# Kernel tuning notes

Measured on AMD Instinct MI355X. Metric: run time of the kernel, lower is better.

## Reference

```python
import jax, jax.numpy as jnp
import numpy as np

MIN_CONF = 0.05          # min_confidence
NMS_IOU = 0.4            # per-class nms iou threshold
POST_IOU = 0.65          # post (cross-class, per-image) nms iou threshold
MAX_OUT = 1000           # nms_max_output_size (also the 'top 1000 boxes' cap)


def _corners(boxes):
    # boxes: [..., 4] (cx, cy, w, h) -> (y1, x1, y2, x2); image w=h=1 since
    # NormalizeBoxes is called without a shape kwarg in the original layer.
    cx, cy, w, h = jnp.moveaxis(boxes, -1, 0)
    return jnp.stack([cy - h / 2, cx - w / 2, cy + h / 2, cx + w / 2], axis=-1)


def _iou_matrix(b):
    # b: [K, 4] (y1, x1, y2, x2) -> [K, K] pairwise IoU
    y1, x1, y2, x2 = b[:, 0], b[:, 1], b[:, 2], b[:, 3]
    area = (y2 - y1) * (x2 - x1)
    ih = jnp.clip(jnp.minimum(y2[:, None], y2[None, :]) - jnp.maximum(y1[:, None], y1[None, :]), 0.0)
    iw = jnp.clip(jnp.minimum(x2[:, None], x2[None, :]) - jnp.maximum(x1[:, None], x1[None, :]), 0.0)
    inter = ih * iw
    union = area[:, None] + area[None, :] - inter
    return inter / jnp.maximum(union, 1e-8)


def _greedy_nms(b, valid, thresh):
    # b: [K,4] corner boxes sorted by descending score; valid: [K] bool.
    # Greedy NMS identical to tf.image.non_max_suppression (suppress IoU > thresh).
    iou = _iou_matrix(b)
    K = b.shape[0]
    idx = jnp.arange(K)
    def body(i, supp):
        active = valid[i] & jnp.logical_not(supp[i])
        return supp | (active & (iou[i] > thresh) & (idx > i))
    supp = jax.lax.fori_loop(0, K, body, jnp.zeros(K, dtype=bool))
    return valid & jnp.logical_not(supp)


def _forward(cls_pred, boxes):
    B, N, C = cls_pred.shape
    K1 = MAX_OUT
    corners = _corners(boxes)                                 # [B, N, 4]

    # --- stage 1: confidence filter + per-(image,class) NMS -----------------
    scores = jnp.transpose(cls_pred, (0, 2, 1))               # [B, C, N]
    masked = jnp.where(scores >= MIN_CONF, scores, -1.0)
    s1, i1 = jax.lax.top_k(masked, K1)                        # [B, C, K1], top-1000 cap
    v1 = s1 >= MIN_CONF
    b1 = jnp.take_along_axis(corners[:, None], i1[..., None], axis=2)  # [B, C, K1, 4]
    keep1 = jax.vmap(lambda bb, vv: _greedy_nms(bb, vv, NMS_IOU))(
        b1.reshape(B * C, K1, 4), v1.reshape(B * C, K1)).reshape(B, C, K1)

    # --- stage 2: per-image cross-class post-NMS ----------------------------
    s2 = jnp.where(keep1, s1, -1.0).reshape(B, C * K1)
    cls_ids = jnp.broadcast_to(jnp.arange(C)[None, :, None], (B, C, K1)).reshape(B, C * K1)
    b2 = b1.reshape(B, C * K1, 4)
    i2 = i1.reshape(B, C * K1)

    K2 = MAX_OUT
    s2t, sel = jax.lax.top_k(s2, K2)                          # [B, K2]
    v2 = s2t >= MIN_CONF
    b2t = jnp.take_along_axis(b2, sel[..., None], axis=1)     # [B, K2, 4]
    cls_t = jnp.take_along_axis(cls_ids, sel, axis=1)         # [B, K2]
    orig_t = jnp.take_along_axis(i2, sel, axis=1)             # [B, K2] anchor index
    keep2 = jax.vmap(lambda bb, vv: _greedy_nms(bb, vv, POST_IOU))(b2t, v2)

    # --- compact kept detections to the front, pad with zeros ---------------
    order = jnp.argsort(jnp.logical_not(keep2).astype(jnp.int32), axis=1)  # stable
    keep_s = jnp.take_along_axis(keep2, order, axis=1)
    conf = jnp.where(keep_s, jnp.take_along_axis(s2t, order, axis=1), 0.0)
    cls_f = jnp.where(keep_s, jnp.take_along_axis(cls_t, order, axis=1), 0).astype(jnp.float32)
    oidx = jnp.take_along_axis(orig_t, order, axis=1)
    raw = jnp.take_along_axis(boxes, oidx[..., None], axis=1)  # original (cx,cy,w,h)
    raw = jnp.where(keep_s[..., None], raw, 0.0)
    out = jnp.concatenate([raw, cls_f[..., None], conf[..., None]], axis=-1)  # [B, K2, 6]
    return jax.lax.stop_gradient(out)


def setup_inputs() -> dict:
    key = jax.random.key(0)
    k1, k2 = jax.random.split(key)
    B, N, C = 8, 100000, 10
    cls_pred = jax.random.uniform(k1, (B, N, C), dtype=jnp.float32)
    boxes = jax.random.uniform(k2, (B, N, 4), dtype=jnp.float32)  # (cx, cy, w, h)
    return {"cls_pred": cls_pred, "boxes": boxes}


def reference(cls_pred, boxes):
    return _forward(cls_pred, boxes)
```

## Files before the change

kernel.cpp:

```cpp
#include <hip/hip_runtime.h>
#include <stdint.h>

typedef unsigned int u32;
typedef unsigned long long u64;

#define B_ 8
#define N_ 100000
#define C_ 10
#define K1_ 1000
#define N2_ (C_ * K1_)
#define NBIN 4096
#define CAP 4096
#define CAP_C 2048
#define SEGROWS 256
#define MIN_CONF_F 0.05f
#define NMS_IOU_F 0.4f
#define POST_IOU_F 0.65f
#define T0_F 0.985f

#define TOTAL_F4 (B_ * N_ * C_ / 4)
#define CBLK 512
#define LCAP 1024

#define NTILE 136
#define NB_ 34
#define TPB_ 4

static __device__ __forceinline__ u32 next_pow2_ge(u32 x, u32 lo, u32 hi) {
  u32 n = lo;
  while (n < x && n < hi) n <<= 1;
  return n;
}

#define TILE_ID(rt, w) ((rt) * 16 - (((rt) * ((rt) - 1)) >> 1) + ((w) - (rt)))

__global__ void k_init(u32* __restrict__ cnt, u32* __restrict__ flag) {
  int t = threadIdx.x;
  if (t < B_ * C_) { cnt[t] = 0; flag[t] = 0; }
}

__global__ __launch_bounds__(256) void k_compact(const float* __restrict__ cls,
                                                 u64* __restrict__ cand,
                                                 u32* __restrict__ cnt,
                                                 u32* __restrict__ flag) {
  __shared__ u32 lcnt[B_ * C_];
  __shared__ u32 sbase[B_ * C_];
  __shared__ u32 ltot;
  __shared__ u32 lovf;
  __shared__ u64 ekey[LCAP];
  __shared__ u32 emeta[LCAP];

  const int tid = threadIdx.x;
  if (tid < B_ * C_) lcnt[tid] = 0;
  if (tid == 0) { ltot = 0; lovf = 0; }
  __syncthreads();

  const u32 lo = (u32)blockIdx.x * ((TOTAL_F4 + CBLK - 1) / CBLK);
  u32 hi = lo + ((TOTAL_F4 + CBLK - 1) / CBLK);
  if (hi > TOTAL_F4) hi = TOTAL_F4;

  const float4* p4 = (const float4*)cls;
  for (u32 f = lo + tid; f < hi; f += 256) {
    float4 v = p4[f];
    u32 e = f * 4u;
    float vs[4] = {v.x, v.y, v.z, v.w};
#pragma unroll
    for (int j = 0; j < 4; ++j) {
      float s = vs[j];
      if (s >= T0_F) {
        u32 g = e + (u32)j;
        u32 gi = g / (u32)C_;
        u32 c = g - gi * (u32)C_;
        u32 bi = gi / (u32)N_;
        u32 i = gi - bi * (u32)N_;
        u32 slice = bi * (u32)C_ + c;
        u32 rank = atomicAdd(&lcnt[slice], 1u);
        u32 pos = atomicAdd(&ltot, 1u);
        if (pos < LCAP) {
          ekey[pos] = ((u64)__float_as_uint(s) << 32) | (u32)(~i);
          emeta[pos] = (slice << 16) | rank;
        } else {
          lovf = 1;
        }
      }
    }
  }
  __syncthreads();

  if (lovf) {
    if (tid < B_ * C_) flag[tid] = 1;
  }
  if (tid < B_ * C_) {
    u32 n = lcnt[tid];
    sbase[tid] = n ? atomicAdd(&cnt[tid], n) : 0u;
  }
  __syncthreads();

  u32 tot = ltot;
  if (tot > LCAP) tot = LCAP;
  for (u32 p = tid; p < tot; p += 256) {
    u32 mta = emeta[p];
    u32 slice = mta >> 16;
    u32 rank = mta & 0xFFFFu;
    u32 dst = sbase[slice] + rank;
    if (dst < CAP_C) cand[(size_t)slice * CAP_C + dst] = ekey[p];
  }
}

__device__ __forceinline__ void bitonic_sort_desc(u64* buf, u32 n, int tid,
                                                  int bd) {
  for (u32 kk = 2; kk <= n; kk <<= 1) {
    for (u32 j = kk >> 1; j > 0; j >>= 1) {
      for (u32 t = tid; t < (n >> 1); t += bd) {
        u32 i = ((t & ~(j - 1)) << 1) | (t & (j - 1));
        u32 l = i | j;
        u64 a = buf[i], bb = buf[l];
        bool desc = ((i & kk) == 0);
        if (desc ? (a < bb) : (a > bb)) { buf[i] = bb; buf[l] = a; }
      }
      __syncthreads();
    }
  }
}

__global__ __launch_bounds__(1024) void k_sel(const u64* __restrict__ cand,
                                              const u32* __restrict__ cnt,
                                              u32* __restrict__ flag,
                                              float* __restrict__ score1,
                                              int* __restrict__ idx1) {
  const int slice = blockIdx.x;
  const int tid = threadIdx.x;
  __shared__ u64 buf[CAP_C];

  u32 m = cnt[slice];
  if (flag[slice] || m < (u32)K1_ || m > (u32)CAP_C) {
    if (tid == 0) flag[slice] = 1;
    return;
  }
  const u32 n = next_pow2_ge(m, 1024u, (u32)CAP_C);

  for (u32 i = tid; i < n; i += 1024)
    buf[i] = (i < m) ? cand[(size_t)slice * CAP_C + i] : 0ull;
  __syncthreads();

  bitonic_sort_desc(buf, n, tid, 1024);

  if (tid < K1_) {
    u64 e = buf[tid];
    u32 k = (u32)(e >> 32);
    score1[slice * K1_ + tid] = __uint_as_float(k);
    idx1[slice * K1_ + tid] = (int)(~(u32)e);
  }
}

__global__ __launch_bounds__(256) void k_topk1_fb(const float* __restrict__ cls,
                                                  const u32* __restrict__ flag,
                                                  float* __restrict__ score1,
                                                  int* __restrict__ idx1) {
  const int slice = blockIdx.x;
  if (!flag[slice]) return;
  const int b = slice / C_, c = slice % C_;
  const int tid = threadIdx.x, bd = blockDim.x;

  __shared__ u32 hist[NBIN];
  __shared__ u64 buf[CAP];
  __shared__ int sh_b1;
  __shared__ u32 sh_base, sh_T, sh_cnt;

  for (int i = tid; i < NBIN; i += bd) hist[i] = 0;
  __syncthreads();
  for (int i = tid; i < N_; i += bd) {
    float s = cls[((size_t)b * N_ + i) * C_ + c];
    if (s >= MIN_CONF_F) atomicAdd(&hist[__float_as_uint(s) >> 19], 1u);
  }
  __syncthreads();
  if (tid == 0) {
    u32 cum = 0; int b1 = -1; u32 base = 0;
    for (int bin = NBIN - 1; bin >= 0; --bin) {
      cum += hist[bin];
      if (cum >= (u32)K1_) { b1 = bin; base = cum - hist[bin]; break; }
    }
    sh_b1 = b1; sh_base = base;
    if (b1 < 0) sh_T = 0;
  }
  __syncthreads();
  const int b1 = sh_b1;

  if (b1 >= 0) {
    const u32 base = sh_base;
    for (int i = tid; i < NBIN; i += bd) hist[i] = 0;
    __syncthreads();
    for (int i = tid; i < N_; i += bd) {
      float s = cls[((size_t)b * N_ + i) * C_ + c];
      if (s >= MIN_CONF_F) {
        u32 k = __float_as_uint(s);
        if ((int)(k >> 19) == b1) atomicAdd(&hist[(k >> 7) & 0xFFFu], 1u);
      }
    }
    __syncthreads();
    if (tid == 0) {
      u32 cum = base;
      u32 T = ((u32)b1) << 19;
      for (int bin = NBIN - 1; bin >= 0; --bin) {
        cum += hist[bin];
        if (cum >= (u32)K1_) { T = (((u32)b1) << 19) | (((u32)bin) << 7); break; }
      }
      sh_T = T;
    }
    __syncthreads();
  }

  if (tid == 0) sh_cnt = 0;
  __syncthreads();
  const u32 T = sh_T;
  for (int i = tid; i < N_; i += bd) {
    float s = cls[((size_t)b * N_ + i) * C_ + c];
    if (s >= MIN_CONF_F) {
      u32 k = __float_as_uint(s);
      if (k >= T) {
        u32 pos = atomicAdd(&sh_cnt, 1u);
        if (pos < CAP) buf[pos] = ((u64)k << 32) | (u32)(~(u32)i);
      }
    }
  }
  __syncthreads();
  u32 m = sh_cnt; if (m > CAP) m = CAP;
  for (int i = tid; i < CAP; i += bd)
    if ((u32)i >= m) buf[i] = 0ull;
  __syncthreads();

  for (u32 kk = 2; kk <= CAP; kk <<= 1) {
    for (u32 j = kk >> 1; j > 0; j >>= 1) {
      for (u32 i = tid; i < CAP; i += bd) {
        u32 l = i ^ j;
        if (l > i) {
          u64 a = buf[i], bb = buf[l];
          bool desc = ((i & kk) == 0);
          if (desc ? (a < bb) : (a > bb)) { buf[i] = bb; buf[l] = a; }
        }
      }
      __syncthreads();
    }
  }

  for (int p = tid; p < K1_; p += bd) {
    u64 e = buf[p];
    u32 k = (u32)(e >> 32);
    float s; int oi;
    if (k == 0) { s = -1.0f; oi = 0; }
    else { s = __uint_as_float(k); oi = (int)(~(u32)e); }
    score1[slice * K1_ + p] = s;
    idx1[slice * K1_ + p] = oi;
  }
}


__global__ __launch_bounds__(256) void k_nms_prep(const float* __restrict__ scores_all,
                                                  const int* __restrict__ origs_all,
                                                  const float* __restrict__ boxes,
                                                  int bdiv,
                                                  float4* __restrict__ cor,
                                                  float* __restrict__ areag) {
  const int slice = blockIdx.x;
  const int b = slice / bdiv;
  const float* scores = scores_all + slice * K1_;
  const int* origs = origs_all + slice * K1_;
  const float* bb = boxes + (size_t)b * N_ * 4;
  for (int p = threadIdx.x; p < 1024; p += 256) {
    float s = (p < K1_) ? scores[p] : -1.0f;
    bool v = (s >= MIN_CONF_F);
    float cx = 0.f, cy = 0.f, w = 0.f, h = 0.f;
    if (v) {
      const float4 bp = *(const float4*)(bb + (size_t)origs[p] * 4);
      cx = bp.x; cy = bp.y; w = bp.z; h = bp.w;
    }
    float y1 = cy - h * 0.5f, x1 = cx - w * 0.5f;
    float y2 = cy + h * 0.5f, x2 = cx + w * 0.5f;
    cor[(slice << 10) + p] = make_float4(y1, x1, y2, x2);
    areag[(slice << 10) + p] = (y2 - y1) * (x2 - x1);
  }
}

__global__ __launch_bounds__(256) void k_nms_build(const float4* __restrict__ cor,
                                                   const float* __restrict__ areag,
                                                   float thr,
                                                   u64* __restrict__ maskg) {
  __shared__ float4 box4[1024];
  __shared__ float area[1024];
  const int blk = blockIdx.x;
  const int slice = blk / NB_;
  const int sub = blk - slice * NB_;
  const int tid = threadIdx.x, wave = tid >> 6, lane = tid & 63;

  for (int p = tid; p < 1024; p += 256) {
    box4[p] = cor[(slice << 10) + p];
    area[p] = areag[(slice << 10) + p];
  }
  __syncthreads();

  const float cf = thr;
  const float cnext = __uint_as_float(__float_as_uint(cf) + 1u);
  const double M = ((double)cf + (double)cnext) * 0.5;
  const bool strict = ((__float_as_uint(cf) & 1u) == 0u);

  u64* mg = maskg + (size_t)slice * (NTILE * 64);

  for (int k = wave; k < TPB_; k += 4) {
    const int tt = sub * TPB_ + k;
    if (tt >= NTILE) break;
    int rt = 0, bse = 0;
    while (tt >= bse + (16 - rt)) { bse += 16 - rt; ++rt; }
    const int w = rt + (tt - bse);
    const int row = (rt << 6) | lane;

    const float4 ib = box4[row];
    const float ia = area[row];
    const float4* jcol = &box4[w << 6];
    u32 mhi = 0, mlo = 0;
#pragma unroll 8
    for (int j = 63; j >= 32; --j) {
      const float4 jb = jcol[j];
      const float ja = (jb.z - jb.x) * (jb.w - jb.y);
      float ih = fminf(ib.z, jb.z) - fmaxf(ib.x, jb.x); ih = fmaxf(ih, 0.0f);
      float iw_ = fminf(ib.w, jb.w) - fmaxf(ib.y, jb.y); iw_ = fmaxf(iw_, 0.0f);
      float inter = ih * iw_;
      float den = fmaxf((ia + ja) - inter, 1e-8f);
      bool p_ = strict ? ((double)inter > M * (double)den)
                       : ((double)inter >= M * (double)den);
      mhi = (mhi << 1) | (p_ ? 1u : 0u);
    }
#pragma unroll 8
    for (int j = 31; j >= 0; --j) {
      const float4 jb = jcol[j];
      const float ja = (jb.z - jb.x) * (jb.w - jb.y);
      float ih = fminf(ib.z, jb.z) - fmaxf(ib.x, jb.x); ih = fmaxf(ih, 0.0f);
      float iw_ = fminf(ib.w, jb.w) - fmaxf(ib.y, jb.y); iw_ = fmaxf(iw_, 0.0f);
      float inter = ih * iw_;
      float den = fmaxf((ia + ja) - inter, 1e-8f);
      bool p_ = strict ? ((double)inter > M * (double)den)
                       : ((double)inter >= M * (double)den);
      mlo = (mlo << 1) | (p_ ? 1u : 0u);
    }
    u64 m = ((u64)mhi << 32) | (u64)mlo;
    if (w == rt) m &= (lane == 63) ? 0ull : (~0ull << (lane + 1));
    mg[(tt << 6) + lane] = m;
  }
}

__device__ void scan_core(const u64* __restrict__ mg,
                          const float* __restrict__ scores,
                          u64* __restrict__ keepb) {
  const int tid = threadIdx.x, wv = tid >> 6, lane = tid & 63;

  float s = (tid < K1_) ? scores[tid] : -1.0f;
  const u64 myvalid = __ballot(s >= MIN_CONF_F);

  u64 ext_partial = 0;

#pragma unroll 1
  for (int g = 0; g < 16; ++g) {
    u64 Tg = 0ull;
    if (g <= wv) Tg = mg[(TILE_ID(g, wv) << 6) + lane];
    const u64 nz = __ballot(Tg != 0ull);
    if (wv == g) {
      u64 ext = ext_partial;
      for (int off = 1; off < 64; off <<= 1) {
        u32 lo = (u32)__shfl_xor((int)(u32)ext, off, 64);
        u32 hi = (u32)__shfl_xor((int)(u32)(ext >> 32), off, 64);
        ext |= ((u64)hi << 32) | lo;
      }
      const u32 tlo = (u32)Tg, thi = (u32)(Tg >> 32);
      u64 rem = myvalid & ~ext;
      u64 cand = rem & nz;
      while (cand) {
        int i = __ffsll((long long)cand) - 1;
        cand &= cand - 1;
        if ((rem >> i) & 1ull) {
          u32 rlo = __builtin_amdgcn_readlane(tlo, i);
          u32 rhi = __builtin_amdgcn_readlane(thi, i);
          u64 row = ((u64)rhi << 32) | rlo;
          rem &= ~row;
          cand &= ~row;
        }
      }
      if (lane == 0) keepb[g] = rem;
    }
    __syncthreads();
    if (wv > g) {
      u64 kg = keepb[g];
      if ((kg >> lane) & 1ull) ext_partial |= Tg;
    }
  }
}

__global__ __launch_bounds__(1024) void k_nms_scan1(const u64* __restrict__ maskg,
                                                    const float* __restrict__ score1,
                                                    int* __restrict__ keep1) {
  __shared__ u64 keepb[16];
  const int slice = blockIdx.x;
  scan_core(maskg + (size_t)slice * (NTILE * 64), score1 + slice * K1_, keepb);
  __syncthreads();
  const int p = threadIdx.x;
  if (p < K1_)
    keep1[slice * K1_ + p] = (int)((keepb[p >> 6] >> (p & 63)) & 1ull);
}

__global__ __launch_bounds__(1024) void k_nms_scan2(const u64* __restrict__ maskg,
                                                    const float* __restrict__ sel_score,
                                                    const int* __restrict__ sel_cls,
                                                    const int* __restrict__ sel_orig,
                                                    const float* __restrict__ boxes,
                                                    float* __restrict__ out) {
  __shared__ u64 keepb[16];
  __shared__ short ord[K1_];
  __shared__ int lbase[17];
  __shared__ int ordc;
  const int b = blockIdx.x;
  const int tid = threadIdx.x;
  scan_core(maskg + (size_t)b * (NTILE * 64), sel_score + b * K1_, keepb);
  __syncthreads();

  if (tid == 0) {
    int acc = 0;
    for (int wdx = 0; wdx < 16; ++wdx) {
      lbase[wdx] = acc;
      acc += __popcll(keepb[wdx]);
    }
    lbase[16] = acc;
    ordc = acc;
  }
  __syncthreads();
  if (tid < 16) {
    u64 m = keepb[tid];
    int base = lbase[tid];
    while (m) {
      int bit = __ffsll((long long)m) - 1;
      ord[base++] = (short)((tid << 6) | bit);
      m &= m - 1;
    }
  }
  __syncthreads();

  for (int t = tid; t < K1_ * 6; t += 1024) out[(size_t)b * K1_ * 6 + t] = 0.0f;
  __syncthreads();

  const int cnt = ordc;
  for (int q = tid; q < cnt; q += 1024) {
    int p = ord[q];
    int oi = sel_orig[b * K1_ + p];
    const float4 bp = *(const float4*)(boxes + ((size_t)b * N_ + oi) * 4);
    float* o = out + ((size_t)b * K1_ + q) * 6;
    o[0] = bp.x; o[1] = bp.y; o[2] = bp.z; o[3] = bp.w;
    o[4] = (float)sel_cls[b * K1_ + p];
    o[5] = sel_score[b * K1_ + p];
  }
}

__device__ __forceinline__ void nms_run(const float* __restrict__ scores,
                                        const int* __restrict__ origs,
                                        const float* __restrict__ boxesB,
                                        float thr,
                                        float4* box4, float* area,
                                        u64* mask, u64* validw, u64* keepw) {
  const int tid = threadIdx.x;
  const int wave = tid >> 6, lane = tid & 63;

  {
    const int p = tid;
    float s = (p < K1_) ? scores[p] : -1.0f;
    bool v = (s >= MIN_CONF_F);
    float cx = 0.f, cy = 0.f, w = 0.f, h = 0.f;
    if (v) {
      const float4 bp = *(const float4*)(boxesB + (size_t)origs[p] * 4);
      cx = bp.x; cy = bp.y; w = bp.z; h = bp.w;
    }
    float y1 = cy - h * 0.5f, x1 = cx - w * 0.5f;
    float y2 = cy + h * 0.5f, x2 = cx + w * 0.5f;
    box4[p] = make_float4(y1, x1, y2, x2);
    area[p] = (y2 - y1) * (x2 - x1);
    u64 mb = __ballot(v);
    if (lane == 0) validw[wave] = mb;
  }
  __syncthreads();

  const float cf = thr;
  const float cnext = __uint_as_float(__float_as_uint(cf) + 1u);
  const double M = ((double)cf + (double)cnext) * 0.5;
  const bool strict = ((__float_as_uint(cf) & 1u) == 0u);

  const int ss = wave & 3, qq = wave >> 2;
  int col;
  if (qq == 0) col = ss;
  else if (qq == 1) col = 7 - ss;
  else if (qq == 2) col = 8 + ss;
  else col = 15 - ss;

  u64 vw = validw[tid & 15];
  u64 supp = 0;

  for (int seg = 0; seg < 4; ++seg) {
    const int ibase = seg * SEGROWS;
    const int lim = (K1_ - ibase < SEGROWS) ? (K1_ - ibase) : SEGROWS;
    const int rtg0 = ibase >> 6;
    int ntile = col - rtg0 + 1;
    if (ntile < 0) ntile = 0;
    if (ntile > 4) ntile = 4;

    if (ntile > 0) {
      float4 ib[4];
      float ia[4];
#pragma unroll
      for (int r = 0; r < 4; ++r) {
        if (r < ntile) {
          const int i = ibase + (r << 6) + lane;
          ib[r] = box4[i];
          ia[r] = area[i];
        }
      }
      u32 mhi[4] = {0, 0, 0, 0}, mlo[4] = {0, 0, 0, 0};
      const float4* jcol = &box4[col << 6];

      for (int j = 63; j >= 32; --j) {
        const float4 jb = jcol[j];
        const float ja = (jb.z - jb.x) * (jb.w - jb.y);
#pragma unroll
        for (int r = 0; r < 4; ++r) {
          if (r < ntile) {
            float ih = fminf(ib[r].z, jb.z) - fmaxf(ib[r].x, jb.x);
            ih = fmaxf(ih, 0.0f);
            float iw_ = fminf(ib[r].w, jb.w) - fmaxf(ib[r].y, jb.y);
            iw_ = fmaxf(iw_, 0.0f);
            float inter = ih * iw_;
            float den = fmaxf((ia[r] + ja) - inter, 1e-8f);
            bool p_ = strict ? ((double)inter > M * (double)den)
                             : ((double)inter >= M * (double)den);
            mhi[r] = (mhi[r] << 1) | (p_ ? 1u : 0u);
          }
        }
      }
      for (int j = 31; j >= 0; --j) {
        const float4 jb = jcol[j];
        const float ja = (jb.z - jb.x) * (jb.w - jb.y);
#pragma unroll
        for (int r = 0; r < 4; ++r) {
          if (r < ntile) {
            float ih = fminf(ib[r].z, jb.z) - fmaxf(ib[r].x, jb.x);
            ih = fmaxf(ih, 0.0f);
            float iw_ = fminf(ib[r].w, jb.w) - fmaxf(ib[r].y, jb.y);
            iw_ = fmaxf(iw_, 0.0f);
            float inter = ih * iw_;
            float den = fmaxf((ia[r] + ja) - inter, 1e-8f);
            bool p_ = strict ? ((double)inter > M * (double)den)
                             : ((double)inter >= M * (double)den);
            mlo[r] = (mlo[r] << 1) | (p_ ? 1u : 0u);
          }
        }
      }
#pragma unroll
      for (int r = 0; r < 4; ++r) {
        if (r < ntile) {
          u64 m = ((u64)mhi[r] << 32) | (u64)mlo[r];
          if (rtg0 + r == col)
            m &= (lane == 63) ? 0ull : (~0ull << (lane + 1));
          const int il = (r << 6) | lane;
          mask[il * 16 + (col ^ (il & 15))] = m;
        }
      }
    }
    __syncthreads();

    if (tid < 64) {
      const int l = tid & 15;
      u64 r0 = 0, r1 = 0, r2 = 0, r3 = 0;
      if (l >= ((ibase + 0) >> 6)) r0 = mask[0 * 16 + (l ^ 0)];
      if (l >= ((ibase + 1) >> 6)) r1 = mask[1 * 16 + (l ^ 1)];
      if (l >= ((ibase + 2) >> 6)) r2 = mask[2 * 16 + (l ^ 2)];
      if (l >= ((ibase + 3) >> 6)) r3 = mask[3 * 16 + (l ^ 3)];
      for (int il = 0; il < lim; il += 4) {
        const int i0 = ibase + il;
        const int n0 = (il + 4 < lim) ? il + 4 : il;
        const int n1 = (il + 5 < lim) ? il + 5 : il;
        const int n2 = (il + 6 < lim) ? il + 6 : il;
        const int n3 = (il + 7 < lim) ? il + 7 : il;
        u64 m0 = r0, m1 = r1, m2 = r2, m3 = r3;
        r0 = (l >= ((ibase + n0) >> 6)) ? mask[n0 * 16 + (l ^ (n0 & 15))] : 0ull;
        r1 = (l >= ((ibase + n1) >> 6)) ? mask[n1 * 16 + (l ^ (n1 & 15))] : 0ull;
        r2 = (l >= ((ibase + n2) >> 6)) ? mask[n2 * 16 + (l ^ (n2 & 15))] : 0ull;
        r3 = (l >= ((ibase + n3) >> 6)) ? mask[n3 * 16 + (l ^ (n3 & 15))] : 0ull;
        bool a;
        a = (tid == (i0 >> 6)) && (((vw & ~supp) >> (i0 & 63)) & 1ull);
        if (__any(a)) supp |= m0;
        a = (tid == ((i0 + 1) >> 6)) && (((vw & ~supp) >> ((i0 + 1) & 63)) & 1ull);
        if (__any(a)) supp |= m1;
        a = (tid == ((i0 + 2) >> 6)) && (((vw & ~supp) >> ((i0 + 2) & 63)) & 1ull);
        if (__any(a)) supp |= m2;
        a = (tid == ((i0 + 3) >> 6)) && (((vw & ~supp) >> ((i0 + 3) & 63)) & 1ull);
        if (__any(a)) supp |= m3;
      }
    }
    __syncthreads();
  }

  if (tid < 16) keepw[tid] = vw & ~supp;
}

__global__ __launch_bounds__(1024) void k_nms1(const float* __restrict__ boxes,
                                               const float* __restrict__ score1,
                                               const int* __restrict__ idx1,
                                               int* __restrict__ keep1) {
  __shared__ float4 box4[1024];
  __shared__ float area[1024];
  __shared__ u64 mask[SEGROWS * 16];
  __shared__ u64 validw[16], keepw[16];

  const int slice = blockIdx.x;
  const int b = slice / C_;
  nms_run(score1 + slice * K1_, idx1 + slice * K1_,
          boxes + (size_t)b * N_ * 4, NMS_IOU_F,
          box4, area, mask, validw, keepw);
  __syncthreads();

  const int p = threadIdx.x;
  if (p < K1_)
    keep1[slice * K1_ + p] = (int)((keepw[p >> 6] >> (p & 63)) & 1ull);
}

__global__ __launch_bounds__(1024) void k_nms2_out(const float* __restrict__ boxes,
                                                   const float* __restrict__ sel_score,
                                                   const int* __restrict__ sel_cls,
                                                   const int* __restrict__ sel_orig,
                                                   float* __restrict__ out) {
  __shared__ float4 box4[1024];
  __shared__ float area[1024];
  __shared__ u64 mask[SEGROWS * 16];
  __shared__ u64 validw[16], keepw[16];
  __shared__ short ord[K1_];
  __shared__ int lbase[17];
  __shared__ int ordc;

  const int b = blockIdx.x;
  const int tid = threadIdx.x;
  nms_run(sel_score + b * K1_, sel_orig + b * K1_,
          boxes + (size_t)b * N_ * 4, POST_IOU_F,
          box4, area, mask, validw, keepw);
  __syncthreads();

  if (tid == 0) {
    int acc = 0;
    for (int wdx = 0; wdx < 16; ++wdx) {
      lbase[wdx] = acc;
      acc += __popcll(keepw[wdx]);
    }
    lbase[16] = acc;
    ordc = acc;
  }
  __syncthreads();
  if (tid < 16) {
    u64 m = keepw[tid];
    int base = lbase[tid];
    while (m) {
      int bit = __ffsll((long long)m) - 1;
      ord[base++] = (short)((tid << 6) | bit);
      m &= m - 1;
    }
  }
  __syncthreads();

  for (int t = tid; t < K1_ * 6; t += 1024) out[(size_t)b * K1_ * 6 + t] = 0.0f;
  __syncthreads();

  const int cnt = ordc;
  for (int q = tid; q < cnt; q += 1024) {
    int p = ord[q];
    int oi = sel_orig[b * K1_ + p];
    const float4 bp = *(const float4*)(boxes + ((size_t)b * N_ + oi) * 4);
    float* o = out + ((size_t)b * K1_ + q) * 6;
    o[0] = bp.x; o[1] = bp.y; o[2] = bp.z; o[3] = bp.w;
    o[4] = (float)sel_cls[b * K1_ + p];
    o[5] = sel_score[b * K1_ + p];
  }
}

__device__ __forceinline__ void suffix_select(const u32* __restrict__ hist,
                                              u32* __restrict__ aux,
                                              u32 base, u32 K,
                                              int* out_bin, u32* out_next) {
  const int t = threadIdx.x;
  u32 h0 = hist[4 * t], h1 = hist[4 * t + 1];
  u32 h2 = hist[4 * t + 2], h3 = hist[4 * t + 3];
  aux[t] = h0 + h1 + h2 + h3;
  __syncthreads();
  for (int off = 1; off < 1024; off <<= 1) {
    u32 v = aux[t] + ((t + off < 1024) ? aux[t + off] : 0u);
    __syncthreads();
    aux[t] = v;
    __syncthreads();
  }
  if (t == 0 && base + aux[0] < K) { *out_bin = -1; *out_next = base; }
  u32 up = (t < 1023) ? aux[t + 1] : 0u;
  u32 s3 = h3 + up;
  u32 s2 = h2 + s3;
  u32 s1 = h1 + s2;
  u32 s0 = h0 + s1;
  u32 c0 = base + s0, c1 = base + s1, c2 = base + s2, c3 = base + s3;
  u32 c4 = base + up;
  if (c0 >= K && c1 < K) { *out_bin = 4 * t;     *out_next = c1; }
  if (c1 >= K && c2 < K) { *out_bin = 4 * t + 1; *out_next = c2; }
  if (c2 >= K && c3 < K) { *out_bin = 4 * t + 2; *out_next = c3; }
  if (c3 >= K && c4 < K) { *out_bin = 4 * t + 3; *out_next = c4; }
  __syncthreads();
}

__global__ __launch_bounds__(1024) void k_topk2(const float* __restrict__ score1,
                                                const int* __restrict__ idx1,
                                                const int* __restrict__ keep1,
                                                float* __restrict__ sel_score,
                                                int* __restrict__ sel_cls,
                                                int* __restrict__ sel_orig) {
  const int b = blockIdx.x;
  const int tid = threadIdx.x;

  __shared__ u32 hist[NBIN];
  __shared__ u32 aux[1024];
  __shared__ u64 buf[CAP];
  __shared__ int sh_bin;
  __shared__ u32 sh_next;
  __shared__ u32 sh_T, sh_cnt;

  for (int i = tid; i < NBIN; i += 1024) hist[i] = 0;
  __syncthreads();
  for (int f = tid; f < N2_; f += 1024) {
    if (keep1[b * N2_ + f])
      atomicAdd(&hist[__float_as_uint(score1[b * N2_ + f]) >> 19], 1u);
  }
  __syncthreads();
  suffix_select(hist, aux, 0u, (u32)K1_, &sh_bin, &sh_next);
  const int b1 = sh_bin;
  const u32 base = sh_next;

  if (b1 >= 0) {
    for (int i = tid; i < NBIN; i += 1024) hist[i] = 0;
    if (tid == 0) sh_bin = -2;
    __syncthreads();
    for (int f = tid; f < N2_; f += 1024) {
      if (keep1[b * N2_ + f]) {
        u32 k = __float_as_uint(score1[b * N2_ + f]);
        if ((int)(k >> 19) == b1) atomicAdd(&hist[(k >> 7) & 0xFFFu], 1u);
      }
    }
    __syncthreads();
    suffix_select(hist, aux, base, (u32)K1_, &sh_bin, &sh_next);
    if (tid == 0) {
      int b2 = sh_bin;
      sh_T = (b2 >= 0) ? ((((u32)b1) << 19) | (((u32)b2) << 7))
                       : (((u32)b1) << 19);
    }
  } else {
    if (tid == 0) sh_T = 0;
  }
  if (tid == 0) sh_cnt = 0;
  __syncthreads();

  const u32 T = sh_T;
  for (int f = tid; f < N2_; f += 1024) {
    if (keep1[b * N2_ + f]) {
      u32 k = __float_as_uint(score1[b * N2_ + f]);
      if (k >= T) {
        u32 pos = atomicAdd(&sh_cnt, 1u);
        if (pos < CAP) buf[pos] = ((u64)k << 32) | (u32)(~(u32)f);
      }
    }
  }
  __syncthreads();
  u32 m = sh_cnt; if (m > CAP) m = CAP;
  const u32 n = next_pow2_ge(m, 1024u, (u32)CAP);
  for (u32 i = tid; i < n; i += 1024)
    if (i >= m) buf[i] = 0ull;
  __syncthreads();

  bitonic_sort_desc(buf, n, tid, 1024);

  if (tid < K1_) {
    u64 e = buf[tid];
    u32 k = (u32)(e >> 32);
    float s; int cls, orig;
    if (k == 0) { s = -1.0f; cls = 0; orig = 0; }
    else {
      s = __uint_as_float(k);
      u32 f = ~(u32)e;
      cls = (int)(f / K1_);
      int slot = (int)(f - (u32)cls * K1_);
      orig = idx1[(b * C_ + cls) * K1_ + slot];
    }
    sel_score[b * K1_ + tid] = s;
    sel_cls[b * K1_ + tid] = cls;
    sel_orig[b * K1_ + tid] = orig;
  }
}

extern "C" void kernel_launch(void* const* d_in, const int* in_sizes, int n_in,
                              void* d_out, int out_size, void* d_ws, size_t ws_size,
                              hipStream_t stream) {
  const float* cls = (const float*)d_in[0];
  const float* boxes = (const float*)d_in[1];
  float* out = (float*)d_out;

  char* ws = (char*)d_ws;
  float* score1    = (float*)(ws);
  int*   idx1      = (int*)(ws + 320000);
  int*   keep1     = (int*)(ws + 640000);
  float* sel_score = (float*)(ws + 960000);
  int*   sel_cls   = (int*)(ws + 992000);
  int*   sel_orig  = (int*)(ws + 1024000);
  u32*   cnt       = (u32*)(ws + 1056000);
  u32*   flag      = (u32*)(ws + 1056320);
  u64*   cand      = (u64*)(ws + 1056640);
  u64*    mask1 = (u64*)(ws + 2367488);
  u64*    mask2 = (u64*)(ws + 7938048);
  float4* cor1  = (float4*)(ws + 8495104);
  float*  area1 = (float*)(ws + 9805824);
  float4* cor2  = (float4*)(ws + 10133504);
  float*  area2 = (float*)(ws + 10264576);
  const size_t WS_NEED = 10297344;

  hipLaunchKernelGGL(k_init, dim3(1), dim3(256), 0, stream, cnt, flag);
  hipLaunchKernelGGL(k_compact, dim3(CBLK), dim3(256), 0, stream,
                     cls, cand, cnt, flag);
  hipLaunchKernelGGL(k_sel, dim3(B_ * C_), dim3(1024), 0, stream,
                     cand, cnt, flag, score1, idx1);
  hipLaunchKernelGGL(k_topk1_fb, dim3(B_ * C_), dim3(256), 0, stream,
                     cls, flag, score1, idx1);

  if (ws_size >= WS_NEED) {
    hipLaunchKernelGGL(k_nms_prep, dim3(B_ * C_), dim3(256), 0, stream,
                       score1, idx1, boxes, C_, cor1, area1);
    hipLaunchKernelGGL(k_nms_build, dim3(B_ * C_ * NB_), dim3(256), 0, stream,
                       cor1, area1, NMS_IOU_F, mask1);
    hipLaunchKernelGGL(k_nms_scan1, dim3(B_ * C_), dim3(1024), 0, stream,
                       mask1, score1, keep1);
    hipLaunchKernelGGL(k_topk2, dim3(B_), dim3(1024), 0, stream,
                       score1, idx1, keep1, sel_score, sel_cls, sel_orig);
    hipLaunchKernelGGL(k_nms_prep, dim3(B_), dim3(256), 0, stream,
                       sel_score, sel_orig, boxes, 1, cor2, area2);
    hipLaunchKernelGGL(k_nms_build, dim3(B_ * NB_), dim3(256), 0, stream,
                       cor2, area2, POST_IOU_F, mask2);
    hipLaunchKernelGGL(k_nms_scan2, dim3(B_), dim3(1024), 0, stream,
                       mask2, sel_score, sel_cls, sel_orig, boxes, out);
  } else {
    hipLaunchKernelGGL(k_nms1, dim3(B_ * C_), dim3(1024), 0, stream,
                       boxes, score1, idx1, keep1);
    hipLaunchKernelGGL(k_topk2, dim3(B_), dim3(1024), 0, stream,
                       score1, idx1, keep1, sel_score, sel_cls, sel_orig);
    hipLaunchKernelGGL(k_nms2_out, dim3(B_), dim3(1024), 0, stream,
                       boxes, sel_score, sel_cls, sel_orig, out);
  }
}
```

Measured before the change: 233.1 us.

## Drop init and prep kernels via per-block segments and fused box prep

Compaction now writes each block's candidates to a private segment with a per-block prefix header instead of using global atomics, so the separate init kernel goes away. The selection kernel gathers those segments with a prefix scan and falls back to the histogram top-k path inside the same kernel, so the fallback launch is removed. Box corner and area computation is fused into the mask-build kernel, which removes the prep launches and their intermediate buffers. The cost is that the gather in k_sel is serial per thread, and every build block recomputes the corners.

```diff
diff --git a/kernel.cpp b/kernel.cpp
--- a/kernel.cpp
+++ b/kernel.cpp
@@ -21,6 +21,7 @@
 #define TOTAL_F4 (B_ * N_ * C_ / 4)
 #define CBLK 512
 #define LCAP 1024
+#define HDRW 84
 
 #define NTILE 136
 #define NB_ 34
@@ -34,28 +35,23 @@
 
 #define TILE_ID(rt, w) ((rt) * 16 - (((rt) * ((rt) - 1)) >> 1) + ((w) - (rt)))
 
-__global__ void k_init(u32* __restrict__ cnt, u32* __restrict__ flag) {
-  int t = threadIdx.x;
-  if (t < B_ * C_) { cnt[t] = 0; flag[t] = 0; }
-}
-
 __global__ __launch_bounds__(256) void k_compact(const float* __restrict__ cls,
                                                  u64* __restrict__ cand,
-                                                 u32* __restrict__ cnt,
-                                                 u32* __restrict__ flag) {
+                                                 u32* __restrict__ hdr) {
   __shared__ u32 lcnt[B_ * C_];
-  __shared__ u32 sbase[B_ * C_];
+  __shared__ u32 lpre[B_ * C_ + 1];
   __shared__ u32 ltot;
   __shared__ u32 lovf;
   __shared__ u64 ekey[LCAP];
   __shared__ u32 emeta[LCAP];
 
   const int tid = threadIdx.x;
+  const u32 bk = blockIdx.x;
   if (tid < B_ * C_) lcnt[tid] = 0;
   if (tid == 0) { ltot = 0; lovf = 0; }
   __syncthreads();
 
-  const u32 lo = (u32)blockIdx.x * ((TOTAL_F4 + CBLK - 1) / CBLK);
+  const u32 lo = bk * ((TOTAL_F4 + CBLK - 1) / CBLK);
   u32 hi = lo + ((TOTAL_F4 + CBLK - 1) / CBLK);
   if (hi > TOTAL_F4) hi = TOTAL_F4;
 
@@ -87,24 +83,30 @@
   }
   __syncthreads();
 
-  if (lovf) {
-    if (tid < B_ * C_) flag[tid] = 1;
-  }
-  if (tid < B_ * C_) {
-    u32 n = lcnt[tid];
-    sbase[tid] = n ? atomicAdd(&cnt[tid], n) : 0u;
-  }
-  __syncthreads();
+  if (tid < B_ * C_) lpre[tid + 1] = lcnt[tid];
+  if (tid == 0) lpre[0] = 0;
+  __syncthreads();
+  for (int off = 1; off < B_ * C_; off <<= 1) {
+    u32 v = 0;
+    const bool act = (tid >= off && tid <= B_ * C_);
+    if (act) v = lpre[tid - off];
+    __syncthreads();
+    if (act) lpre[tid] += v;
+    __syncthreads();
+  }
 
   u32 tot = ltot;
   if (tot > LCAP) tot = LCAP;
+  u64* seg = cand + (size_t)bk * LCAP;
   for (u32 p = tid; p < tot; p += 256) {
     u32 mta = emeta[p];
     u32 slice = mta >> 16;
     u32 rank = mta & 0xFFFFu;
-    u32 dst = sbase[slice] + rank;
-    if (dst < CAP_C) cand[(size_t)slice * CAP_C + dst] = ekey[p];
-  }
+    u32 dst = lpre[slice] + rank;
+    if (dst < LCAP) seg[dst] = ekey[p];
+  }
+  if (tid <= B_ * C_) hdr[bk * HDRW + tid] = lpre[tid];
+  if (tid == 0) hdr[bk * HDRW + 81] = lovf;
 }
 
 __device__ __forceinline__ void bitonic_sort_desc(u64* buf, u32 n, int tid,
@@ -123,49 +125,72 @@
   }
 }
 
-__global__ __launch_bounds__(1024) void k_sel(const u64* __restrict__ cand,
-                                              const u32* __restrict__ cnt,
-                                              u32* __restrict__ flag,
+__global__ __launch_bounds__(1024) void k_sel(const float* __restrict__ cls,
+                                              const u64* __restrict__ cand,
+                                              const u32* __restrict__ hdr,
                                               float* __restrict__ score1,
                                               int* __restrict__ idx1) {
   const int slice = blockIdx.x;
   const int tid = threadIdx.x;
-  __shared__ u64 buf[CAP_C];
-
-  u32 m = cnt[slice];
-  if (flag[slice] || m < (u32)K1_ || m > (u32)CAP_C) {
-    if (tid == 0) flag[slice] = 1;
-    return;
-  }
-  const u32 n = next_pow2_ge(m, 1024u, (u32)CAP_C);
-
-  for (u32 i = tid; i < n; i += 1024)
-    buf[i] = (i < m) ? cand[(size_t)slice * CAP_C + i] : 0ull;
-  __syncthreads();
-
-  bitonic_sort_desc(buf, n, tid, 1024);
-
-  if (tid < K1_) {
-    u64 e = buf[tid];
-    u32 k = (u32)(e >> 32);
-    score1[slice * K1_ + tid] = __uint_as_float(k);
-    idx1[slice * K1_ + tid] = (int)(~(u32)e);
-  }
-}
-
-__global__ __launch_bounds__(256) void k_topk1_fb(const float* __restrict__ cls,
-                                                  const u32* __restrict__ flag,
-                                                  float* __restrict__ score1,
-                                                  int* __restrict__ idx1) {
-  const int slice = blockIdx.x;
-  if (!flag[slice]) return;
-  const int b = slice / C_, c = slice % C_;
-  const int tid = threadIdx.x, bd = blockDim.x;
+  const int bd = 1024;
 
   __shared__ u32 hist[NBIN];
   __shared__ u64 buf[CAP];
   __shared__ int sh_b1;
-  __shared__ u32 sh_base, sh_T, sh_cnt;
+  __shared__ u32 sh_base, sh_T, sh_cnt, sh_ovf;
+
+  u32* cnts = hist;
+  u32* starts = hist + 512;
+  u32* pre = hist + 1024;
+
+  if (tid == 0) sh_ovf = 0;
+  __syncthreads();
+  if (tid < CBLK) {
+    const u32* h = hdr + (size_t)tid * HDRW;
+    u32 a = h[slice], b2 = h[slice + 1];
+    starts[tid] = a;
+    cnts[tid] = b2 - a;
+    pre[tid + 1] = b2 - a;
+    if (h[81]) sh_ovf = 1;
+  }
+  if (tid == 0) pre[0] = 0;
+  __syncthreads();
+  for (int off = 1; off < CBLK; off <<= 1) {
+    u32 v = 0;
+    const bool act = (tid >= off && tid <= CBLK);
+    if (act) v = pre[tid - off];
+    __syncthreads();
+    if (act) pre[tid] += v;
+    __syncthreads();
+  }
+  const u32 m = pre[CBLK];
+  const bool fast = (sh_ovf == 0) && m >= (u32)K1_ && m <= (u32)CAP_C;
+
+  if (fast) {
+    if (tid < CBLK) {
+      u32 n = cnts[tid];
+      u32 base = pre[tid];
+      const u64* src = cand + (size_t)tid * LCAP + starts[tid];
+      for (u32 r = 0; r < n; ++r) buf[base + r] = src[r];
+    }
+    __syncthreads();
+    const u32 nn = next_pow2_ge(m, 1024u, (u32)CAP_C);
+    for (u32 i2 = tid; i2 < nn; i2 += bd)
+      if (i2 >= m) buf[i2] = 0ull;
+    __syncthreads();
+
+    bitonic_sort_desc(buf, nn, tid, bd);
+
+    if (tid < K1_) {
+      u64 e = buf[tid];
+      u32 k = (u32)(e >> 32);
+      score1[slice * K1_ + tid] = __uint_as_float(k);
+      idx1[slice * K1_ + tid] = (int)(~(u32)e);
+    }
+    return;
+  }
+
+  const int b = slice / C_, c = slice % C_;
 
   for (int i = tid; i < NBIN; i += bd) hist[i] = 0;
   __syncthreads();
@@ -224,9 +249,9 @@
     }
   }
   __syncthreads();
-  u32 m = sh_cnt; if (m > CAP) m = CAP;
+  u32 mm = sh_cnt; if (mm > CAP) mm = CAP;
   for (int i = tid; i < CAP; i += bd)
-    if ((u32)i >= m) buf[i] = 0ull;
+    if ((u32)i >= mm) buf[i] = 0ull;
   __syncthreads();
 
   for (u32 kk = 2; kk <= CAP; kk <<= 1) {
@@ -234,9 +259,9 @@
       for (u32 i = tid; i < CAP; i += bd) {
         u32 l = i ^ j;
         if (l > i) {
-          u64 a = buf[i], bb = buf[l];
+          u64 a = buf[i], bb2 = buf[l];
           bool desc = ((i & kk) == 0);
-          if (desc ? (a < bb) : (a > bb)) { buf[i] = bb; buf[l] = a; }
+          if (desc ? (a < bb2) : (a > bb2)) { buf[i] = bb2; buf[l] = a; }
         }
       }
       __syncthreads();
@@ -255,18 +280,23 @@
 }
 
 
-__global__ __launch_bounds__(256) void k_nms_prep(const float* __restrict__ scores_all,
-                                                  const int* __restrict__ origs_all,
-                                                  const float* __restrict__ boxes,
-                                                  int bdiv,
-                                                  float4* __restrict__ cor,
-                                                  float* __restrict__ areag) {
-  const int slice = blockIdx.x;
+__global__ __launch_bounds__(256) void k_nms_build(const float* __restrict__ scores_all,
+                                                   const int* __restrict__ origs_all,
+                                                   const float* __restrict__ boxes,
+                                                   int bdiv, float thr,
+                                                   u64* __restrict__ maskg) {
+  __shared__ float4 box4[1024];
+  __shared__ float area[1024];
+  const int blk = blockIdx.x;
+  const int slice = blk / NB_;
+  const int sub = blk - slice * NB_;
   const int b = slice / bdiv;
   const float* scores = scores_all + slice * K1_;
   const int* origs = origs_all + slice * K1_;
   const float* bb = boxes + (size_t)b * N_ * 4;
-  for (int p = threadIdx.x; p < 1024; p += 256) {
+  const int tid = threadIdx.x, wave = tid >> 6, lane = tid & 63;
+
+  for (int p = tid; p < 1024; p += 256) {
     float s = (p < K1_) ? scores[p] : -1.0f;
     bool v = (s >= MIN_CONF_F);
     float cx = 0.f, cy = 0.f, w = 0.f, h = 0.f;
@@ -276,25 +306,8 @@
     }
     float y1 = cy - h * 0.5f, x1 = cx - w * 0.5f;
     float y2 = cy + h * 0.5f, x2 = cx + w * 0.5f;
-    cor[(slice << 10) + p] = make_float4(y1, x1, y2, x2);
-    areag[(slice << 10) + p] = (y2 - y1) * (x2 - x1);
-  }
-}
-
-__global__ __launch_bounds__(256) void k_nms_build(const float4* __restrict__ cor,
-                                                   const float* __restrict__ areag,
-                                                   float thr,
-                                                   u64* __restrict__ maskg) {
-  __shared__ float4 box4[1024];
-  __shared__ float area[1024];
-  const int blk = blockIdx.x;
-  const int slice = blk / NB_;
-  const int sub = blk - slice * NB_;
-  const int tid = threadIdx.x, wave = tid >> 6, lane = tid & 63;
-
-  for (int p = tid; p < 1024; p += 256) {
-    box4[p] = cor[(slice << 10) + p];
-    area[p] = areag[(slice << 10) + p];
+    box4[p] = make_float4(y1, x1, y2, x2);
+    area[p] = (y2 - y1) * (x2 - x1);
   }
   __syncthreads();
 
@@ -812,38 +825,26 @@
   float* sel_score = (float*)(ws + 960000);
   int*   sel_cls   = (int*)(ws + 992000);
   int*   sel_orig  = (int*)(ws + 1024000);
-  u32*   cnt       = (u32*)(ws + 1056000);
-  u32*   flag      = (u32*)(ws + 1056320);
-  u64*   cand      = (u64*)(ws + 1056640);
-  u64*    mask1 = (u64*)(ws + 2367488);
-  u64*    mask2 = (u64*)(ws + 7938048);
-  float4* cor1  = (float4*)(ws + 8495104);
-  float*  area1 = (float*)(ws + 9805824);
-  float4* cor2  = (float4*)(ws + 10133504);
-  float*  area2 = (float*)(ws + 10264576);
-  const size_t WS_NEED = 10297344;
-
-  hipLaunchKernelGGL(k_init, dim3(1), dim3(256), 0, stream, cnt, flag);
+  u32*   hdr       = (u32*)(ws + 1056000);
+  u64*   cand      = (u64*)(ws + 1228032);
+  u64*   mask1     = (u64*)(ws + 5422336);
+  u64*   mask2     = (u64*)(ws + 10992896);
+  const size_t WS_NEED = 11549952;
+
   hipLaunchKernelGGL(k_compact, dim3(CBLK), dim3(256), 0, stream,
-                     cls, cand, cnt, flag);
+                     cls, cand, hdr);
   hipLaunchKernelGGL(k_sel, dim3(B_ * C_), dim3(1024), 0, stream,
-                     cand, cnt, flag, score1, idx1);
-  hipLaunchKernelGGL(k_topk1_fb, dim3(B_ * C_), dim3(256), 0, stream,
-                     cls, flag, score1, idx1);
+                     cls, cand, hdr, score1, idx1);
 
   if (ws_size >= WS_NEED) {
-    hipLaunchKernelGGL(k_nms_prep, dim3(B_ * C_), dim3(256), 0, stream,
-                       score1, idx1, boxes, C_, cor1, area1);
     hipLaunchKernelGGL(k_nms_build, dim3(B_ * C_ * NB_), dim3(256), 0, stream,
-                       cor1, area1, NMS_IOU_F, mask1);
+                       score1, idx1, boxes, C_, NMS_IOU_F, mask1);
     hipLaunchKernelGGL(k_nms_scan1, dim3(B_ * C_), dim3(1024), 0, stream,
                        mask1, score1, keep1);
     hipLaunchKernelGGL(k_topk2, dim3(B_), dim3(1024), 0, stream,
                        score1, idx1, keep1, sel_score, sel_cls, sel_orig);
-    hipLaunchKernelGGL(k_nms_prep, dim3(B_), dim3(256), 0, stream,
-                       sel_score, sel_orig, boxes, 1, cor2, area2);
     hipLaunchKernelGGL(k_nms_build, dim3(B_ * NB_), dim3(256), 0, stream,
-                       cor2, area2, POST_IOU_F, mask2);
+                       sel_score, sel_orig, boxes, 1, POST_IOU_F, mask2);
     hipLaunchKernelGGL(k_nms_scan2, dim3(B_), dim3(1024), 0, stream,
                        mask2, sel_score, sel_cls, sel_orig, boxes, out);
   } else {
```

After: 237.4 us. No clear change (+1.9%).
